# Kernel optimization log

Measured on AMD Instinct MI355X. Metric: run time of the kernel, lower is better.

The kernel has to match this reference:

```python
import jax, jax.numpy as jnp
import numpy as np

N, E, F_IN = 100000, 600000, 128
HID, NCLS = 128, 2
# ratio=0.8 applied three times: ceil(0.8*100000), ceil(0.8*80000), ceil(0.8*64000)
K1, K2, K3 = 80000, 64000, 51200


def setup_inputs() -> dict:
    key = jax.random.key(0)
    k = jax.random.split(key, 16)
    s = 0.05
    p = {}
    p['x'] = jax.random.normal(k[0], (N, F_IN), dtype=jnp.float32)
    p['edge_index'] = jax.random.randint(k[1], (2, E), 0, N)
    # GraphConv i: out = lin_rel(sum_j x_j) + lin_root(x_i); lin_root has no bias (PyG)
    p['Wr1'] = jax.random.normal(k[2], (HID, F_IN), jnp.float32) * s
    p['br1'] = jnp.zeros((HID,), jnp.float32)
    p['Wroot1'] = jax.random.normal(k[3], (HID, F_IN), jnp.float32) * s
    p['pw1'] = jax.random.normal(k[4], (HID,), jnp.float32) * s
    p['Wr2'] = jax.random.normal(k[5], (HID, HID), jnp.float32) * s
    p['br2'] = jnp.zeros((HID,), jnp.float32)
    p['Wroot2'] = jax.random.normal(k[6], (HID, HID), jnp.float32) * s
    p['pw2'] = jax.random.normal(k[7], (HID,), jnp.float32) * s
    p['Wr3'] = jax.random.normal(k[8], (HID, HID), jnp.float32) * s
    p['br3'] = jnp.zeros((HID,), jnp.float32)
    p['Wroot3'] = jax.random.normal(k[9], (HID, HID), jnp.float32) * s
    p['pw3'] = jax.random.normal(k[10], (HID,), jnp.float32) * s
    p['W_lin1'] = jax.random.normal(k[11], (HID, 2 * HID), jnp.float32) * s
    p['b_lin1'] = jnp.zeros((HID,), jnp.float32)
    p['W_lin2'] = jax.random.normal(k[12], (64, HID), jnp.float32) * s
    p['b_lin2'] = jnp.zeros((64,), jnp.float32)
    p['W_lin3'] = jax.random.normal(k[13], (NCLS, 64), jnp.float32) * s
    p['b_lin3'] = jnp.zeros((NCLS,), jnp.float32)
    return p


def _gconv(x, src, dst, emask, Wr, br, Wroot):
    # PyG GraphConv(aggr='add'): masked edges contribute zero (== removed edge)
    msg = x[src] * emask[:, None].astype(x.dtype)           # [E, F]
    agg = jax.ops.segment_sum(msg, dst, num_segments=x.shape[0])
    return agg @ Wr.T + br + x @ Wroot.T


def _topk_pool(x, src, dst, emask, w, k):
    # PyG TopKPooling: score = tanh((x.w)/||w||); keep top-k nodes; x = x[perm]*score[perm]
    score = jnp.tanh((x @ w) / jnp.linalg.norm(w))
    vals, perm = jax.lax.top_k(score, k)
    x_new = x[perm] * vals[:, None]
    new_idx = jnp.full((x.shape[0],), -1, jnp.int32).at[perm].set(
        jnp.arange(k, dtype=jnp.int32))
    ns, nd = new_idx[src], new_idx[dst]
    valid = emask & (ns >= 0) & (nd >= 0)
    return x_new, jnp.where(valid, ns, 0), jnp.where(valid, nd, 0), valid


def _readout(x):
    # single graph (batch=None): gmp || gap -> [1, 2F]
    return jnp.concatenate([x.max(axis=0), x.mean(axis=0)])[None, :]


def reference(x, edge_index, Wr1, br1, Wroot1, pw1, Wr2, br2, Wroot2, pw2,
              Wr3, br3, Wroot3, pw3, W_lin1, b_lin1, W_lin2, b_lin2, W_lin3, b_lin3):
    src = edge_index[0].astype(jnp.int32)
    dst = edge_index[1].astype(jnp.int32)
    emask = jnp.ones((src.shape[0],), dtype=bool)

    h = jax.nn.relu(_gconv(x, src, dst, emask, Wr1, br1, Wroot1))
    h, src, dst, emask = _topk_pool(h, src, dst, emask, pw1, K1)
    r1 = _readout(h)

    h = jax.nn.relu(_gconv(h, src, dst, emask, Wr2, br2, Wroot2))
    h, src, dst, emask = _topk_pool(h, src, dst, emask, pw2, K2)
    r2 = _readout(h)

    h = jax.nn.relu(_gconv(h, src, dst, emask, Wr3, br3, Wroot3))
    h, src, dst, emask = _topk_pool(h, src, dst, emask, pw3, K3)
    r3 = _readout(h)

    z = r1 + r2 + r3                                        # [1, 256]
    z = jax.nn.relu(z @ W_lin1.T + b_lin1)                  # dropout: inference no-op
    z = jax.nn.relu(z @ W_lin2.T + b_lin2)
    return z @ W_lin3.T + b_lin3                            # [1, num_classes]
```

## Files before the change

kernel.cpp:

```cpp
#include <hip/hip_runtime.h>
#include <hip/hip_bf16.h>
#include <math.h>

#define N0 100000
#define E0 600000
#define KP1 80000
#define KP2 64000
#define KP3 51200
#define F 128
#define RPB 2048
#define RMID 128
#define SCAN_CHUNK 1024
#define NCHUNK ((N0 + SCAN_CHUNK - 1) / SCAN_CHUNK)

typedef __attribute__((ext_vector_type(8))) short short8;
typedef __attribute__((ext_vector_type(4))) float f32x4;

__device__ __forceinline__ unsigned fkey(float f) {
    unsigned u = __float_as_uint(f);
    return u ^ ((u & 0x80000000u) ? 0xFFFFFFFFu : 0x80000000u);
}
__device__ __forceinline__ unsigned short f2b(float f) {
    __hip_bfloat16 h = __float2bfloat16(f);
    return *(unsigned short*)&h;
}
__device__ __forceinline__ float b2f(unsigned short u) {
    __hip_bfloat16 h;
    *(unsigned short*)&h = u;
    return __bfloat162float(h);
}

__global__ __launch_bounds__(256) void cvt4K(const float* __restrict__ in,
                                             unsigned short* __restrict__ out, int n4) {
    int i = blockIdx.x * 256 + threadIdx.x;
    if (i >= n4) return;
    float4 v = *(const float4*)(in + (size_t)i * 4);
    *(ushort4*)(out + (size_t)i * 4) = make_ushort4(f2b(v.x), f2b(v.y), f2b(v.z), f2b(v.w));
}

__global__ __launch_bounds__(256) void cvtWAllK(const float* __restrict__ a0, const float* __restrict__ a1,
                                                const float* __restrict__ a2, const float* __restrict__ a3,
                                                const float* __restrict__ a4, const float* __restrict__ a5,
                                                unsigned short* __restrict__ o) {
    int m = blockIdx.y;
    const float* src = (m == 0) ? a0 : (m == 1) ? a1 : (m == 2) ? a2 : (m == 3) ? a3 : (m == 4) ? a4 : a5;
    int i = blockIdx.x * 256 + threadIdx.x;
    float4 v = *(const float4*)(src + (size_t)i * 4);
    *(ushort4*)(o + (size_t)m * 16384 + (size_t)i * 4) = make_ushort4(f2b(v.x), f2b(v.y), f2b(v.z), f2b(v.w));
}

__global__ __launch_bounds__(256) void histDstK(const int* __restrict__ dst, unsigned* __restrict__ cnt) {
    int e = blockIdx.x * 256 + threadIdx.x;
    if (e < E0) atomicAdd(&cnt[dst[e]], 1u);
}

__global__ __launch_bounds__(256) void scanReduceK(const unsigned* __restrict__ cnt,
                                                   unsigned* __restrict__ chunkSum, int nbins) {
    __shared__ unsigned sh[256];
    int base = blockIdx.x * SCAN_CHUNK + threadIdx.x * 4;
    unsigned s = 0;
#pragma unroll
    for (int i = 0; i < 4; i++) { int b = base + i; if (b < nbins) s += cnt[b]; }
    sh[threadIdx.x] = s;
    __syncthreads();
    for (int off = 128; off; off >>= 1) {
        if (threadIdx.x < off) sh[threadIdx.x] += sh[threadIdx.x + off];
        __syncthreads();
    }
    if (threadIdx.x == 0) chunkSum[blockIdx.x] = sh[0];
}

__global__ void scanChunksK(const unsigned* __restrict__ chunkSum, unsigned* __restrict__ chunkOff,
                            int nchunks, unsigned* __restrict__ totalOut) {
    if (threadIdx.x == 0) {
        unsigned run = 0;
        for (int i = 0; i < nchunks; i++) { chunkOff[i] = run; run += chunkSum[i]; }
        *totalOut = run;
    }
}

__global__ __launch_bounds__(256) void scanFinalK(const unsigned* __restrict__ cnt,
                                                  const unsigned* __restrict__ chunkOff,
                                                  unsigned* __restrict__ rowptr, int nbins) {
    __shared__ unsigned sh[256];
    int t = threadIdx.x;
    int base = blockIdx.x * SCAN_CHUNK + t * 4;
    unsigned c[4], s = 0;
#pragma unroll
    for (int i = 0; i < 4; i++) { int b = base + i; c[i] = (b < nbins) ? cnt[b] : 0u; s += c[i]; }
    sh[t] = s;
    __syncthreads();
    for (int off = 1; off < 256; off <<= 1) {
        unsigned v = (t >= off) ? sh[t - off] : 0u;
        __syncthreads();
        sh[t] += v;
        __syncthreads();
    }
    unsigned basep = chunkOff[blockIdx.x] + sh[t] - s;
#pragma unroll
    for (int i = 0; i < 4; i++) {
        int b = base + i;
        if (b < nbins) { rowptr[b] = basep; basep += c[i]; }
    }
}

__global__ __launch_bounds__(256) void scatterFillK(const int* __restrict__ src,
                                                    const int* __restrict__ dst,
                                                    const unsigned* __restrict__ rowptr,
                                                    unsigned* __restrict__ fill,
                                                    int* __restrict__ sortedSrc) {
    int e = blockIdx.x * 256 + threadIdx.x;
    if (e >= E0) return;
    int d = dst[e];
    unsigned p = rowptr[d] + atomicAdd(&fill[d], 1u);
    sortedSrc[p] = src[e];
}

__global__ __launch_bounds__(256) void iotaK(int* o, int n) {
    int i = blockIdx.x * 256 + threadIdx.x;
    if (i < n) o[i] = i;
}

__global__ __launch_bounds__(256) void aggSegB(const unsigned short* __restrict__ x,
                                               const int* __restrict__ srcCur,
                                               const unsigned* __restrict__ rowptr,
                                               const int* __restrict__ orig,
                                               unsigned short* __restrict__ agg, int n) {
    int g = blockIdx.x * 8 + (threadIdx.x >> 5);
    int q = threadIdx.x & 31;
    if (g >= n) return;
    int d = orig[g];
    unsigned e0 = rowptr[d], e1 = rowptr[d + 1];
    float a0 = 0.f, a1 = 0.f, a2 = 0.f, a3 = 0.f;
    for (unsigned e = e0; e < e1; e++) {
        int s = srcCur[e];
        if (s < 0) continue;
        ushort4 v = *(const ushort4*)(x + (size_t)s * F + q * 4);
        a0 += b2f(v.x); a1 += b2f(v.y); a2 += b2f(v.z); a3 += b2f(v.w);
    }
    *(ushort4*)(agg + (size_t)g * F + q * 4) = make_ushort4(f2b(a0), f2b(a1), f2b(a2), f2b(a3));
}

__global__ __launch_bounds__(256) void buildOrigK(const int* __restrict__ origIn,
                                                  const int* __restrict__ nidx,
                                                  int* __restrict__ origOut, int n) {
    int i = blockIdx.x * 256 + threadIdx.x;
    if (i < n) { int ni = nidx[i]; if (ni >= 0) origOut[ni] = origIn[i]; }
}

__global__ __launch_bounds__(256) void remapSrcK(const int* __restrict__ srcIn,
                                                 const int* __restrict__ nidx,
                                                 int* __restrict__ srcOut) {
    int e = blockIdx.x * 256 + threadIdx.x;
    if (e >= E0) return;
    int s = srcIn[e];
    srcOut[e] = (s >= 0) ? nidx[s] : -1;
}

#define CPAD 40
__global__ __launch_bounds__(256) void convM(const unsigned short* __restrict__ A0,
                                             const unsigned short* __restrict__ A1,
                                             const unsigned short* __restrict__ W0,
                                             const unsigned short* __restrict__ W1,
                                             const float* __restrict__ br,
                                             float* __restrict__ out, int n) {
    __shared__ unsigned short As[128 * CPAD];
    __shared__ unsigned short Bs[128 * CPAD];
    int tid = threadIdx.x;
    int w = tid >> 6, l = tid & 63;
    int r = l & 15, g = l >> 4;
    int bm = blockIdx.x * 128;
    int srow = tid >> 2, q4 = tid & 3;

    f32x4 acc[2][8];
#pragma unroll
    for (int m = 0; m < 2; m++)
#pragma unroll
        for (int c = 0; c < 8; c++) acc[m][c] = (f32x4){0.f, 0.f, 0.f, 0.f};

    for (int ph = 0; ph < 2; ph++) {
        const unsigned short* A = ph ? A1 : A0;
        const unsigned short* W = ph ? W1 : W0;
        for (int kk = 0; kk < 128; kk += 32) {
            __syncthreads();
#pragma unroll
            for (int h2 = 0; h2 < 2; h2++) {
                int rr = srow + h2 * 64;
                uint4 av = make_uint4(0u, 0u, 0u, 0u);
                if (bm + rr < n) av = *(const uint4*)(A + (size_t)(bm + rr) * F + kk + q4 * 8);
                *(uint4*)(&As[rr * CPAD + q4 * 8]) = av;
                uint4 wv = *(const uint4*)(W + (size_t)rr * F + kk + q4 * 8);
                *(uint4*)(&Bs[rr * CPAD + q4 * 8]) = wv;
            }
            __syncthreads();
            short8 af[2], bf[8];
#pragma unroll
            for (int m = 0; m < 2; m++)
                af[m] = *(const short8*)(&As[(w * 32 + m * 16 + r) * CPAD + g * 8]);
#pragma unroll
            for (int c = 0; c < 8; c++)
                bf[c] = *(const short8*)(&Bs[(c * 16 + r) * CPAD + g * 8]);
#pragma unroll
            for (int m = 0; m < 2; m++)
#pragma unroll
                for (int c = 0; c < 8; c++)
                    acc[m][c] = __builtin_amdgcn_mfma_f32_16x16x32_bf16(af[m], bf[c], acc[m][c], 0, 0, 0);
        }
    }

#pragma unroll
    for (int c = 0; c < 8; c++) {
        int col = c * 16 + r;
        float bias = br[col];
#pragma unroll
        for (int m = 0; m < 2; m++) {
#pragma unroll
            for (int j = 0; j < 4; j++) {
                int row = bm + w * 32 + m * 16 + g * 4 + j;
                if (row < n) out[(size_t)row * F + col] = fmaxf(acc[m][c][j] + bias, 0.f);
            }
        }
    }
}

__global__ __launch_bounds__(256) void scoreK(const float* __restrict__ h,
                                              const float* __restrict__ pw,
                                              float* __restrict__ sc,
                                              unsigned* __restrict__ keys, int n) {
    int wv = threadIdx.x >> 6, lane = threadIdx.x & 63;
    int row = blockIdx.x * 4 + wv;
    if (row >= n) return;
    float p0 = pw[lane], p1 = pw[lane + 64];
    float h0 = h[(size_t)row * F + lane], h1 = h[(size_t)row * F + lane + 64];
    float d = h0 * p0 + h1 * p1;
    float q = p0 * p0 + p1 * p1;
    for (int off = 32; off; off >>= 1) {
        d += __shfl_down(d, off);
        q += __shfl_down(q, off);
    }
    if (lane == 0) {
        float s = tanhf(d / sqrtf(q));
        sc[row] = s;
        keys[row] = fkey(s);
    }
}

__global__ void initSelK(unsigned* hist, unsigned* st, int k) {
    hist[threadIdx.x] = 0;
    if (threadIdx.x == 0) { st[0] = 0u; st[1] = (unsigned)k; }
}

__global__ __launch_bounds__(256) void histK(const unsigned* __restrict__ keys, int n,
                                             int p, const unsigned* __restrict__ st,
                                             unsigned* __restrict__ hist) {
    __shared__ unsigned lh[256];
    lh[threadIdx.x] = 0;
    __syncthreads();
    unsigned prefix = st[0];
    int i = blockIdx.x * 256 + threadIdx.x;
    if (i < n) {
        unsigned key = keys[i];
        bool m = (p == 0) || ((key >> (32 - 8 * p)) == (prefix >> (32 - 8 * p)));
        if (m) atomicAdd(&lh[(key >> (24 - 8 * p)) & 255u], 1u);
    }
    __syncthreads();
    if (lh[threadIdx.x]) atomicAdd(&hist[threadIdx.x], lh[threadIdx.x]);
}

__global__ void selectK(unsigned* hist, unsigned* st, int p) {
    __shared__ unsigned h[256];
    h[threadIdx.x] = hist[threadIdx.x];
    __syncthreads();
    if (threadIdx.x == 0) {
        unsigned krem = st[1], cum = 0;
        for (int b = 255; b >= 0; b--) {
            unsigned c = h[b];
            if (cum + c >= krem) {
                st[0] |= ((unsigned)b) << (24 - 8 * p);
                st[1] = krem - cum;
                break;
            }
            cum += c;
        }
    }
    __syncthreads();
    hist[threadIdx.x] = 0;
}

__global__ __launch_bounds__(256) void countsK(const unsigned* __restrict__ keys, int n,
                                               const unsigned* __restrict__ st,
                                               int* __restrict__ bGT, int* __restrict__ bEQ) {
    __shared__ int cg_, ce_;
    if (threadIdx.x == 0) { cg_ = 0; ce_ = 0; }
    __syncthreads();
    unsigned t = st[0];
    int g = 0, e = 0;
    for (int it = 0; it < 4; it++) {
        int i = blockIdx.x * 1024 + it * 256 + threadIdx.x;
        if (i < n) {
            unsigned k = keys[i];
            g += (k > t);
            e += (k == t);
        }
    }
    atomicAdd(&cg_, g);
    atomicAdd(&ce_, e);
    __syncthreads();
    if (threadIdx.x == 0) { bGT[blockIdx.x] = cg_; bEQ[blockIdx.x] = ce_; }
}

__global__ void scanK(const int* bGT, const int* bEQ, int* sGT, int* sEQ, int nb) {
    if (threadIdx.x == 0 && blockIdx.x == 0) {
        int g = 0, e = 0;
        for (int b = 0; b < nb; b++) {
            sGT[b] = g; sEQ[b] = e;
            g += bGT[b]; e += bEQ[b];
        }
    }
}

__global__ __launch_bounds__(256) void markK(const unsigned* __restrict__ keys, int n,
                                             const unsigned* __restrict__ st,
                                             const int* __restrict__ sGT,
                                             const int* __restrict__ sEQ,
                                             int* __restrict__ nidx) {
    __shared__ int wG[4], wE[4];
    __shared__ int runG, runE;
    int tid = threadIdx.x, wv = tid >> 6, lane = tid & 63;
    if (tid == 0) { runG = 0; runE = 0; }
    unsigned t = st[0];
    int needEq = (int)st[1];
    int gOff = sGT[blockIdx.x], eOff = sEQ[blockIdx.x];
    unsigned long long mlt = (((unsigned long long)1) << lane) - 1ull;
    __syncthreads();
    for (int it = 0; it < 4; it++) {
        int i = blockIdx.x * 1024 + it * 256 + tid;
        bool inb = i < n;
        unsigned k = inb ? keys[i] : 0u;
        bool pG = inb && (k > t), pE = inb && (k == t);
        unsigned long long bG = __ballot(pG), bE = __ballot(pE);
        int lpG = __popcll(bG & mlt), lpE = __popcll(bE & mlt);
        if (lane == 0) { wG[wv] = __popcll(bG); wE[wv] = __popcll(bE); }
        __syncthreads();
        int woG = 0, woE = 0;
        for (int w = 0; w < wv; w++) { woG += wG[w]; woE += wE[w]; }
        int gB = gOff + runG + woG + lpG;
        int eB = eOff + runE + woE + lpE;
        int ni = -1;
        if (pG) ni = gB + (eB < needEq ? eB : needEq);
        else if (pE && eB < needEq) ni = gB + eB;
        if (inb) nidx[i] = ni;
        __syncthreads();
        if (tid == 0) {
            runG += wG[0] + wG[1] + wG[2] + wG[3];
            runE += wE[0] + wE[1] + wE[2] + wE[3];
        }
        __syncthreads();
    }
}

__global__ __launch_bounds__(256) void gatherB(const float* __restrict__ h,
                                               const float* __restrict__ sc,
                                               const int* __restrict__ nidx,
                                               unsigned short* __restrict__ out, int n) {
    int t = blockIdx.x * 256 + threadIdx.x;
    int i = t >> 5, q = t & 31;
    if (i >= n) return;
    int ni = nidx[i];
    if (ni < 0) return;
    float s = sc[i];
    float4 v = *(const float4*)(h + (size_t)i * F + q * 4);
    *(ushort4*)(out + (size_t)ni * F + q * 4) =
        make_ushort4(f2b(v.x * s), f2b(v.y * s), f2b(v.z * s), f2b(v.w * s));
}

__global__ __launch_bounds__(128) void rpartK(const unsigned short* __restrict__ x, int k,
                                              float* __restrict__ pmax, float* __restrict__ psum) {
    int f = threadIdx.x;
    float m = -INFINITY, s = 0.f;
    for (int row = blockIdx.x; row < k; row += gridDim.x) {
        float v = b2f(x[(size_t)row * F + f]);
        m = fmaxf(m, v);
        s += v;
    }
    pmax[(size_t)blockIdx.x * F + f] = m;
    psum[(size_t)blockIdx.x * F + f] = s;
}

__global__ __launch_bounds__(128) void rmidK(const float* __restrict__ pmax,
                                             const float* __restrict__ psum,
                                             float* __restrict__ mmax,
                                             float* __restrict__ msum) {
    int f = threadIdx.x;
    int b0 = blockIdx.x * (RPB / RMID);
    float m = -INFINITY, s = 0.f;
#pragma unroll
    for (int i = 0; i < RPB / RMID; i++) {
        m = fmaxf(m, pmax[(size_t)(b0 + i) * F + f]);
        s += psum[(size_t)(b0 + i) * F + f];
    }
    mmax[(size_t)blockIdx.x * F + f] = m;
    msum[(size_t)blockIdx.x * F + f] = s;
}

__global__ __launch_bounds__(128) void rfinalK(const float* __restrict__ mmax,
                                               const float* __restrict__ msum, int k,
                                               float* __restrict__ r) {
    int f = threadIdx.x;
    float m = -INFINITY, s = 0.f;
    for (int b = 0; b < RMID; b++) {
        m = fmaxf(m, mmax[(size_t)b * F + f]);
        s += msum[(size_t)b * F + f];
    }
    r[f] += m;
    r[F + f] += s / (float)k;
}

__global__ __launch_bounds__(256) void mlpK(const float* __restrict__ r,
                                            const float* __restrict__ W1, const float* __restrict__ b1,
                                            const float* __restrict__ W2, const float* __restrict__ b2,
                                            const float* __restrict__ W3, const float* __restrict__ b3,
                                            float* __restrict__ out) {
    __shared__ float z0[256], z1[128], z2[64];
    int t = threadIdx.x;
    z0[t] = r[t];
    __syncthreads();
    if (t < 128) {
        float a = b1[t];
        for (int kk = 0; kk < 256; kk++) a = fmaf(W1[t * 256 + kk], z0[kk], a);
        z1[t] = fmaxf(a, 0.f);
    }
    __syncthreads();
    if (t < 64) {
        float a = b2[t];
        for (int kk = 0; kk < 128; kk++) a = fmaf(W2[t * 128 + kk], z1[kk], a);
        z2[t] = fmaxf(a, 0.f);
    }
    __syncthreads();
    if (t < 2) {
        float a = b3[t];
        for (int kk = 0; kk < 64; kk++) a = fmaf(W3[t * 64 + kk], z2[kk], a);
        out[t] = a;
    }
}

extern "C" void kernel_launch(void* const* d_in, const int* in_sizes, int n_in,
                              void* d_out, int out_size, void* d_ws, size_t ws_size,
                              hipStream_t stream) {
    const float* x = (const float*)d_in[0];
    const int* ei = (const int*)d_in[1];
    const float* Wr[3]    = { (const float*)d_in[2],  (const float*)d_in[6],  (const float*)d_in[10] };
    const float* br[3]    = { (const float*)d_in[3],  (const float*)d_in[7],  (const float*)d_in[11] };
    const float* Wroot[3] = { (const float*)d_in[4],  (const float*)d_in[8],  (const float*)d_in[12] };
    const float* pw[3]    = { (const float*)d_in[5],  (const float*)d_in[9],  (const float*)d_in[13] };
    const float* W1 = (const float*)d_in[14];
    const float* b1 = (const float*)d_in[15];
    const float* W2 = (const float*)d_in[16];
    const float* b2 = (const float*)d_in[17];
    const float* W3 = (const float*)d_in[18];
    const float* b3 = (const float*)d_in[19];
    float* out = (float*)d_out;
    char* w = (char*)d_ws;

    size_t o = 0;
    auto alc = [&](size_t bytes) { size_t r = o; o += (bytes + 255) & ~(size_t)255; return r; };
    float*          bufA   = (float*)(w + alc((size_t)N0 * F * 4));
    unsigned short* xbf    = (unsigned short*)(w + alc((size_t)N0 * F * 2));
    unsigned short* aggbf  = (unsigned short*)(w + alc((size_t)N0 * F * 2));
    unsigned short* bufBbf = (unsigned short*)(w + alc((size_t)KP1 * F * 2));
    unsigned short* wbf    = (unsigned short*)(w + alc((size_t)6 * 16384 * 2));
    float*    sc     = (float*)(w + alc((size_t)N0 * 4));
    unsigned* keys   = (unsigned*)(w + alc((size_t)N0 * 4));
    int*      nidx   = (int*)(w + alc((size_t)N0 * 4));
    int*      sSrc0  = (int*)(w + alc((size_t)E0 * 4));
    int*      srcCA  = (int*)(w + alc((size_t)E0 * 4));
    int*      srcCB  = (int*)(w + alc((size_t)E0 * 4));
    unsigned* cnt    = (unsigned*)(w + alc((size_t)N0 * 4));
    unsigned* rowptr = (unsigned*)(w + alc((size_t)(N0 + 1) * 4));
    int*      origA  = (int*)(w + alc((size_t)N0 * 4));
    int*      origB  = (int*)(w + alc((size_t)N0 * 4));
    unsigned* chS    = (unsigned*)(w + alc(NCHUNK * 4));
    unsigned* chO    = (unsigned*)(w + alc(NCHUNK * 4));
    unsigned* hist   = (unsigned*)(w + alc(256 * 4));
    unsigned* st     = (unsigned*)(w + alc(64));
    int*      bGT    = (int*)(w + alc(128 * 4));
    int*      bEQ    = (int*)(w + alc(128 * 4));
    int*      sGT    = (int*)(w + alc(128 * 4));
    int*      sEQ    = (int*)(w + alc(128 * 4));
    float*    r      = (float*)(w + alc(256 * 4));
    float*    pmax   = (float*)(w + alc((size_t)RPB * F * 4));
    float*    psum   = (float*)(w + alc((size_t)RPB * F * 4));
    float*    mmax   = (float*)(w + alc((size_t)RMID * F * 4));
    float*    msum   = (float*)(w + alc((size_t)RMID * F * 4));
    if (o > ws_size) return;

    const int* srcOrig = ei;
    const int* dstOrig = ei + E0;

    cvt4K<<<(N0 * F / 4 + 255) / 256, 256, 0, stream>>>(x, xbf, N0 * F / 4);
    cvtWAllK<<<dim3(16, 6), 256, 0, stream>>>(Wr[0], Wroot[0], Wr[1], Wroot[1], Wr[2], Wroot[2], wbf);

    hipMemsetAsync(cnt, 0, (size_t)N0 * 4, stream);
    histDstK<<<(E0 + 255) / 256, 256, 0, stream>>>(dstOrig, cnt);
    scanReduceK<<<NCHUNK, 256, 0, stream>>>(cnt, chS, N0);
    scanChunksK<<<1, 1, 0, stream>>>(chS, chO, NCHUNK, rowptr + N0);
    scanFinalK<<<NCHUNK, 256, 0, stream>>>(cnt, chO, rowptr, N0);
    hipMemsetAsync(cnt, 0, (size_t)N0 * 4, stream);
    scatterFillK<<<(E0 + 255) / 256, 256, 0, stream>>>(srcOrig, dstOrig, rowptr, cnt, sSrc0);
    iotaK<<<(N0 + 255) / 256, 256, 0, stream>>>(origA, N0);

    hipMemsetAsync(r, 0, 256 * 4, stream);

    const int ns[3] = { N0, KP1, KP2 };
    const int ks[3] = { KP1, KP2, KP3 };
    const int* srcCur[3] = { sSrc0, srcCA, srcCB };
    int* srcNext[3] = { srcCA, srcCB, nullptr };
    const int* origCur[3] = { origA, origB, origA };
    int* origNext[3] = { origB, origA, nullptr };

    for (int L = 0; L < 3; L++) {
        int n = ns[L], k = ks[L];
        const unsigned short* xinbf = (L == 0) ? xbf : bufBbf;

        aggSegB<<<(n + 7) / 8, 256, 0, stream>>>(xinbf, srcCur[L], rowptr, origCur[L], aggbf, n);
        convM<<<(n + 127) / 128, 256, 0, stream>>>(aggbf, xinbf,
                                                   wbf + (size_t)(L * 2) * 16384,
                                                   wbf + (size_t)(L * 2 + 1) * 16384,
                                                   br[L], bufA, n);
        scoreK<<<(n + 3) / 4, 256, 0, stream>>>(bufA, pw[L], sc, keys, n);

        initSelK<<<1, 256, 0, stream>>>(hist, st, k);
        for (int p = 0; p < 4; p++) {
            histK<<<(n + 255) / 256, 256, 0, stream>>>(keys, n, p, st, hist);
            selectK<<<1, 256, 0, stream>>>(hist, st, p);
        }
        int nb = (n + 1023) / 1024;
        countsK<<<nb, 256, 0, stream>>>(keys, n, st, bGT, bEQ);
        scanK<<<1, 1, 0, stream>>>(bGT, bEQ, sGT, sEQ, nb);
        markK<<<nb, 256, 0, stream>>>(keys, n, st, sGT, sEQ, nidx);

        gatherB<<<(n * 32 + 255) / 256, 256, 0, stream>>>(bufA, sc, nidx, bufBbf, n);
        if (L < 2) {
            buildOrigK<<<(n + 255) / 256, 256, 0, stream>>>(origCur[L], nidx, origNext[L], n);
            remapSrcK<<<(E0 + 255) / 256, 256, 0, stream>>>(srcCur[L], nidx, srcNext[L]);
        }

        rpartK<<<RPB, 128, 0, stream>>>(bufBbf, k, pmax, psum);
        rmidK<<<RMID, 128, 0, stream>>>(pmax, psum, mmax, msum);
        rfinalK<<<1, 128, 0, stream>>>(mmax, msum, k, r);
    }

    mlpK<<<1, 256, 0, stream>>>(r, W1, b1, W2, b2, W3, b3, out);
}
```

Measured before the change: 668.6 us.

## Fuse scoring into conv epilogue, merge select passes, widen aggregation loads

The top-k score (dot with a pre-normalized pool weight, then tanh) is computed inside the MFMA conv epilogue, and the hidden state is now stored as bf16 instead of fp32, so the separate score kernel and half the activation traffic go away. The histogram and select kernels are merged using a last-block-done atomic counter, and the block scan is folded into countsK the same way, which removes several tiny launches per layer. Aggregation now uses 8-wide bf16 loads with a 4-edge unrolled loop, and the gather kernel reads bf16. The risks are extra bf16 rounding of h before pooling, and correctness that depends on the threadfence/atomic last-block pattern.

```diff
diff --git a/kernel.cpp b/kernel.cpp
--- a/kernel.cpp
+++ b/kernel.cpp
@@ -14,6 +14,7 @@
 #define NCHUNK ((N0 + SCAN_CHUNK - 1) / SCAN_CHUNK)
 
 typedef __attribute__((ext_vector_type(8))) short short8;
+typedef __attribute__((ext_vector_type(8))) unsigned short ushort8;
 typedef __attribute__((ext_vector_type(4))) float f32x4;
 
 __device__ __forceinline__ unsigned fkey(float f) {
@@ -47,6 +48,21 @@
     int i = blockIdx.x * 256 + threadIdx.x;
     float4 v = *(const float4*)(src + (size_t)i * 4);
     *(ushort4*)(o + (size_t)m * 16384 + (size_t)i * 4) = make_ushort4(f2b(v.x), f2b(v.y), f2b(v.z), f2b(v.w));
+}
+
+__global__ __launch_bounds__(128) void pwnK(const float* __restrict__ p0, const float* __restrict__ p1,
+                                            const float* __restrict__ p2, float* __restrict__ pwn) {
+    __shared__ float sh[128];
+    int l = blockIdx.x, t = threadIdx.x;
+    const float* p = (l == 0) ? p0 : (l == 1) ? p1 : p2;
+    float v = p[t];
+    sh[t] = v * v;
+    __syncthreads();
+    for (int off = 64; off; off >>= 1) {
+        if (t < off) sh[t] += sh[t + off];
+        __syncthreads();
+    }
+    pwn[l * 128 + t] = v / sqrtf(sh[0]);
 }
 
 __global__ __launch_bounds__(256) void histDstK(const int* __restrict__ dst, unsigned* __restrict__ cnt) {
@@ -126,19 +142,42 @@
                                                const unsigned* __restrict__ rowptr,
                                                const int* __restrict__ orig,
                                                unsigned short* __restrict__ agg, int n) {
-    int g = blockIdx.x * 8 + (threadIdx.x >> 5);
-    int q = threadIdx.x & 31;
+    int g = blockIdx.x * 16 + (threadIdx.x >> 4);
+    int q = threadIdx.x & 15;
     if (g >= n) return;
     int d = orig[g];
     unsigned e0 = rowptr[d], e1 = rowptr[d + 1];
-    float a0 = 0.f, a1 = 0.f, a2 = 0.f, a3 = 0.f;
-    for (unsigned e = e0; e < e1; e++) {
+    float a[8];
+#pragma unroll
+    for (int j = 0; j < 8; j++) a[j] = 0.f;
+    unsigned e = e0;
+    for (; e + 4 <= e1; e += 4) {
+        int s0 = srcCur[e], s1 = srcCur[e + 1], s2 = srcCur[e + 2], s3 = srcCur[e + 3];
+        ushort8 v0 = *(const ushort8*)(x + (size_t)(s0 < 0 ? 0 : s0) * F + q * 8);
+        ushort8 v1 = *(const ushort8*)(x + (size_t)(s1 < 0 ? 0 : s1) * F + q * 8);
+        ushort8 v2 = *(const ushort8*)(x + (size_t)(s2 < 0 ? 0 : s2) * F + q * 8);
+        ushort8 v3 = *(const ushort8*)(x + (size_t)(s3 < 0 ? 0 : s3) * F + q * 8);
+        float m0 = s0 < 0 ? 0.f : 1.f, m1 = s1 < 0 ? 0.f : 1.f;
+        float m2 = s2 < 0 ? 0.f : 1.f, m3 = s3 < 0 ? 0.f : 1.f;
+#pragma unroll
+        for (int j = 0; j < 8; j++) {
+            a[j] = fmaf(b2f(v0[j]), m0, a[j]);
+            a[j] = fmaf(b2f(v1[j]), m1, a[j]);
+            a[j] = fmaf(b2f(v2[j]), m2, a[j]);
+            a[j] = fmaf(b2f(v3[j]), m3, a[j]);
+        }
+    }
+    for (; e < e1; e++) {
         int s = srcCur[e];
         if (s < 0) continue;
-        ushort4 v = *(const ushort4*)(x + (size_t)s * F + q * 4);
-        a0 += b2f(v.x); a1 += b2f(v.y); a2 += b2f(v.z); a3 += b2f(v.w);
-    }
-    *(ushort4*)(agg + (size_t)g * F + q * 4) = make_ushort4(f2b(a0), f2b(a1), f2b(a2), f2b(a3));
+        ushort8 v = *(const ushort8*)(x + (size_t)s * F + q * 8);
+#pragma unroll
+        for (int j = 0; j < 8; j++) a[j] += b2f(v[j]);
+    }
+    ushort8 o;
+#pragma unroll
+    for (int j = 0; j < 8; j++) o[j] = f2b(a[j]);
+    *(ushort8*)(agg + (size_t)g * F + q * 8) = o;
 }
 
 __global__ __launch_bounds__(256) void buildOrigK(const int* __restrict__ origIn,
@@ -163,7 +202,10 @@
                                              const unsigned short* __restrict__ W0,
                                              const unsigned short* __restrict__ W1,
                                              const float* __restrict__ br,
-                                             float* __restrict__ out, int n) {
+                                             const float* __restrict__ pwn,
+                                             unsigned short* __restrict__ hbf,
+                                             float* __restrict__ sc,
+                                             unsigned* __restrict__ keys, int n) {
     __shared__ unsigned short As[128 * CPAD];
     __shared__ unsigned short Bs[128 * CPAD];
     int tid = threadIdx.x;
@@ -208,73 +250,86 @@
         }
     }
 
+    float pd[2][4];
+#pragma unroll
+    for (int m = 0; m < 2; m++)
+#pragma unroll
+        for (int j = 0; j < 4; j++) pd[m][j] = 0.f;
+
 #pragma unroll
     for (int c = 0; c < 8; c++) {
         int col = c * 16 + r;
         float bias = br[col];
+        float pwc = pwn[col];
 #pragma unroll
         for (int m = 0; m < 2; m++) {
 #pragma unroll
             for (int j = 0; j < 4; j++) {
                 int row = bm + w * 32 + m * 16 + g * 4 + j;
-                if (row < n) out[(size_t)row * F + col] = fmaxf(acc[m][c][j] + bias, 0.f);
+                float h = fmaxf(acc[m][c][j] + bias, 0.f);
+                pd[m][j] += h * pwc;
+                if (row < n) hbf[(size_t)row * F + col] = f2b(h);
             }
         }
     }
-}
-
-__global__ __launch_bounds__(256) void scoreK(const float* __restrict__ h,
-                                              const float* __restrict__ pw,
-                                              float* __restrict__ sc,
-                                              unsigned* __restrict__ keys, int n) {
-    int wv = threadIdx.x >> 6, lane = threadIdx.x & 63;
-    int row = blockIdx.x * 4 + wv;
-    if (row >= n) return;
-    float p0 = pw[lane], p1 = pw[lane + 64];
-    float h0 = h[(size_t)row * F + lane], h1 = h[(size_t)row * F + lane + 64];
-    float d = h0 * p0 + h1 * p1;
-    float q = p0 * p0 + p1 * p1;
-    for (int off = 32; off; off >>= 1) {
-        d += __shfl_down(d, off);
-        q += __shfl_down(q, off);
-    }
-    if (lane == 0) {
-        float s = tanhf(d / sqrtf(q));
-        sc[row] = s;
-        keys[row] = fkey(s);
-    }
-}
-
-__global__ void initSelK(unsigned* hist, unsigned* st, int k) {
+#pragma unroll
+    for (int m = 0; m < 2; m++) {
+#pragma unroll
+        for (int j = 0; j < 4; j++) {
+            float p = pd[m][j];
+            p += __shfl_xor(p, 1);
+            p += __shfl_xor(p, 2);
+            p += __shfl_xor(p, 4);
+            p += __shfl_xor(p, 8);
+            if (r == 0) {
+                int row = bm + w * 32 + m * 16 + g * 4 + j;
+                if (row < n) {
+                    float s = tanhf(p);
+                    sc[row] = s;
+                    keys[row] = fkey(s);
+                }
+            }
+        }
+    }
+}
+
+__global__ void initSelK(unsigned* hist, unsigned* st, unsigned* done, unsigned* done2, int k) {
     hist[threadIdx.x] = 0;
-    if (threadIdx.x == 0) { st[0] = 0u; st[1] = (unsigned)k; }
-}
-
-__global__ __launch_bounds__(256) void histK(const unsigned* __restrict__ keys, int n,
-                                             int p, const unsigned* __restrict__ st,
-                                             unsigned* __restrict__ hist) {
+    if (threadIdx.x == 0) { st[0] = 0u; st[1] = (unsigned)k; *done = 0u; *done2 = 0u; }
+}
+
+__global__ __launch_bounds__(256) void histSelK(const unsigned* __restrict__ keys, int n,
+                                                int p, unsigned* __restrict__ st,
+                                                unsigned* __restrict__ hist,
+                                                unsigned* __restrict__ done, int nb) {
     __shared__ unsigned lh[256];
-    lh[threadIdx.x] = 0;
+    __shared__ bool last;
+    int tid = threadIdx.x;
+    lh[tid] = 0;
     __syncthreads();
     unsigned prefix = st[0];
-    int i = blockIdx.x * 256 + threadIdx.x;
+    int i = blockIdx.x * 256 + tid;
     if (i < n) {
         unsigned key = keys[i];
         bool m = (p == 0) || ((key >> (32 - 8 * p)) == (prefix >> (32 - 8 * p)));
         if (m) atomicAdd(&lh[(key >> (24 - 8 * p)) & 255u], 1u);
     }
     __syncthreads();
-    if (lh[threadIdx.x]) atomicAdd(&hist[threadIdx.x], lh[threadIdx.x]);
-}
-
-__global__ void selectK(unsigned* hist, unsigned* st, int p) {
-    __shared__ unsigned h[256];
-    h[threadIdx.x] = hist[threadIdx.x];
-    __syncthreads();
-    if (threadIdx.x == 0) {
+    if (lh[tid]) atomicAdd(&hist[tid], lh[tid]);
+    __syncthreads();
+    if (tid == 0) {
+        __threadfence();
+        last = (atomicAdd(done, 1u) == (unsigned)(nb - 1));
+    }
+    __syncthreads();
+    if (!last) return;
+    lh[tid] = atomicAdd(&hist[tid], 0u);
+    __syncthreads();
+    hist[tid] = 0;
+    if (tid == 0) {
         unsigned krem = st[1], cum = 0;
         for (int b = 255; b >= 0; b--) {
-            unsigned c = h[b];
+            unsigned c = lh[b];
             if (cum + c >= krem) {
                 st[0] |= ((unsigned)b) << (24 - 8 * p);
                 st[1] = krem - cum;
@@ -282,21 +337,24 @@
             }
             cum += c;
         }
-    }
-    __syncthreads();
-    hist[threadIdx.x] = 0;
+        *done = 0u;
+    }
 }
 
 __global__ __launch_bounds__(256) void countsK(const unsigned* __restrict__ keys, int n,
                                                const unsigned* __restrict__ st,
-                                               int* __restrict__ bGT, int* __restrict__ bEQ) {
+                                               int* __restrict__ bGT, int* __restrict__ bEQ,
+                                               int* __restrict__ sGT, int* __restrict__ sEQ,
+                                               unsigned* __restrict__ done2, int nb) {
     __shared__ int cg_, ce_;
-    if (threadIdx.x == 0) { cg_ = 0; ce_ = 0; }
+    __shared__ bool last;
+    int tid = threadIdx.x;
+    if (tid == 0) { cg_ = 0; ce_ = 0; }
     __syncthreads();
     unsigned t = st[0];
     int g = 0, e = 0;
     for (int it = 0; it < 4; it++) {
-        int i = blockIdx.x * 1024 + it * 256 + threadIdx.x;
+        int i = blockIdx.x * 1024 + it * 256 + tid;
         if (i < n) {
             unsigned k = keys[i];
             g += (k > t);
@@ -306,16 +364,22 @@
     atomicAdd(&cg_, g);
     atomicAdd(&ce_, e);
     __syncthreads();
-    if (threadIdx.x == 0) { bGT[blockIdx.x] = cg_; bEQ[blockIdx.x] = ce_; }
-}
-
-__global__ void scanK(const int* bGT, const int* bEQ, int* sGT, int* sEQ, int nb) {
-    if (threadIdx.x == 0 && blockIdx.x == 0) {
-        int g = 0, e = 0;
+    if (tid == 0) {
+        bGT[blockIdx.x] = cg_;
+        bEQ[blockIdx.x] = ce_;
+        __threadfence();
+        last = (atomicAdd(done2, 1u) == (unsigned)(nb - 1));
+    }
+    __syncthreads();
+    if (!last) return;
+    if (tid == 0) {
+        int gs = 0, es = 0;
         for (int b = 0; b < nb; b++) {
-            sGT[b] = g; sEQ[b] = e;
-            g += bGT[b]; e += bEQ[b];
-        }
+            sGT[b] = gs; sEQ[b] = es;
+            gs += atomicAdd(&bGT[b], 0);
+            es += atomicAdd(&bEQ[b], 0);
+        }
+        *done2 = 0u;
     }
 }
 
@@ -359,19 +423,21 @@
     }
 }
 
-__global__ __launch_bounds__(256) void gatherB(const float* __restrict__ h,
+__global__ __launch_bounds__(256) void gatherB(const unsigned short* __restrict__ h,
                                                const float* __restrict__ sc,
                                                const int* __restrict__ nidx,
                                                unsigned short* __restrict__ out, int n) {
     int t = blockIdx.x * 256 + threadIdx.x;
-    int i = t >> 5, q = t & 31;
+    int i = t >> 4, q = t & 15;
     if (i >= n) return;
     int ni = nidx[i];
     if (ni < 0) return;
     float s = sc[i];
-    float4 v = *(const float4*)(h + (size_t)i * F + q * 4);
-    *(ushort4*)(out + (size_t)ni * F + q * 4) =
-        make_ushort4(f2b(v.x * s), f2b(v.y * s), f2b(v.z * s), f2b(v.w * s));
+    ushort8 v = *(const ushort8*)(h + (size_t)i * F + q * 8);
+    ushort8 o;
+#pragma unroll
+    for (int j = 0; j < 8; j++) o[j] = f2b(b2f(v[j]) * s);
+    *(ushort8*)(out + (size_t)ni * F + q * 8) = o;
 }
 
 __global__ __launch_bounds__(128) void rpartK(const unsigned short* __restrict__ x, int k,
@@ -464,11 +530,12 @@
 
     size_t o = 0;
     auto alc = [&](size_t bytes) { size_t r = o; o += (bytes + 255) & ~(size_t)255; return r; };
-    float*          bufA   = (float*)(w + alc((size_t)N0 * F * 4));
+    unsigned short* hbf    = (unsigned short*)(w + alc((size_t)N0 * F * 2));
     unsigned short* xbf    = (unsigned short*)(w + alc((size_t)N0 * F * 2));
     unsigned short* aggbf  = (unsigned short*)(w + alc((size_t)N0 * F * 2));
     unsigned short* bufBbf = (unsigned short*)(w + alc((size_t)KP1 * F * 2));
     unsigned short* wbf    = (unsigned short*)(w + alc((size_t)6 * 16384 * 2));
+    float*    pwn    = (float*)(w + alc(3 * 128 * 4));
     float*    sc     = (float*)(w + alc((size_t)N0 * 4));
     unsigned* keys   = (unsigned*)(w + alc((size_t)N0 * 4));
     int*      nidx   = (int*)(w + alc((size_t)N0 * 4));
@@ -483,6 +550,8 @@
     unsigned* chO    = (unsigned*)(w + alc(NCHUNK * 4));
     unsigned* hist   = (unsigned*)(w + alc(256 * 4));
     unsigned* st     = (unsigned*)(w + alc(64));
+    unsigned* done   = (unsigned*)(w + alc(64));
+    unsigned* done2  = (unsigned*)(w + alc(64));
     int*      bGT    = (int*)(w + alc(128 * 4));
     int*      bEQ    = (int*)(w + alc(128 * 4));
     int*      sGT    = (int*)(w + alc(128 * 4));
@@ -499,6 +568,7 @@
 
     cvt4K<<<(N0 * F / 4 + 255) / 256, 256, 0, stream>>>(x, xbf, N0 * F / 4);
     cvtWAllK<<<dim3(16, 6), 256, 0, stream>>>(Wr[0], Wroot[0], Wr[1], Wroot[1], Wr[2], Wroot[2], wbf);
+    pwnK<<<3, 128, 0, stream>>>(pw[0], pw[1], pw[2], pwn);
 
     hipMemsetAsync(cnt, 0, (size_t)N0 * 4, stream);
     histDstK<<<(E0 + 255) / 256, 256, 0, stream>>>(dstOrig, cnt);
@@ -522,24 +592,21 @@
         int n = ns[L], k = ks[L];
         const unsigned short* xinbf = (L == 0) ? xbf : bufBbf;
 
-        aggSegB<<<(n + 7) / 8, 256, 0, stream>>>(xinbf, srcCur[L], rowptr, origCur[L], aggbf, n);
+        aggSegB<<<(n + 15) / 16, 256, 0, stream>>>(xinbf, srcCur[L], rowptr, origCur[L], aggbf, n);
         convM<<<(n + 127) / 128, 256, 0, stream>>>(aggbf, xinbf,
                                                    wbf + (size_t)(L * 2) * 16384,
                                                    wbf + (size_t)(L * 2 + 1) * 16384,
-                                                   br[L], bufA, n);
-        scoreK<<<(n + 3) / 4, 256, 0, stream>>>(bufA, pw[L], sc, keys, n);
-
-        initSelK<<<1, 256, 0, stream>>>(hist, st, k);
-        for (int p = 0; p < 4; p++) {
-            histK<<<(n + 255) / 256, 256, 0, stream>>>(keys, n, p, st, hist);
-            selectK<<<1, 256, 0, stream>>>(hist, st, p);
-        }
+                                                   br[L], pwn + L * 128, hbf, sc, keys, n);
+
+        initSelK<<<1, 256, 0, stream>>>(hist, st, done, done2, k);
+        int nbh = (n + 255) / 256;
+        for (int p = 0; p < 4; p++)
+            histSelK<<<nbh, 256, 0, stream>>>(keys, n, p, st, hist, done, nbh);
         int nb = (n + 1023) / 1024;
-        countsK<<<nb, 256, 0, stream>>>(keys, n, st, bGT, bEQ);
-        scanK<<<1, 1, 0, stream>>>(bGT, bEQ, sGT, sEQ, nb);
+        countsK<<<nb, 256, 0, stream>>>(keys, n, st, bGT, bEQ, sGT, sEQ, done2, nb);
         markK<<<nb, 256, 0, stream>>>(keys, n, st, sGT, sEQ, nidx);
 
-        gatherB<<<(n * 32 + 255) / 256, 256, 0, stream>>>(bufA, sc, nidx, bufBbf, n);
+        gatherB<<<(n * 16 + 255) / 256, 256, 0, stream>>>(hbf, sc, nidx, bufBbf, n);
         if (L < 2) {
             buildOrigK<<<(n + 255) / 256, 256, 0, stream>>>(origCur[L], nidx, origNext[L], n);
             remapSrcK<<<(E0 + 255) / 256, 256, 0, stream>>>(srcCur[L], nidx, srcNext[L]);
```

After: 640.1 us. -4.3%, faster.
